# Kernel optimization log

Hardware: AMD Instinct MI355X
Metric: run time of the kernel (lower is better)

The kernel has to match this reference:

```python
import jax, jax.numpy as jnp
import numpy as np

N_TOKENS = 8192
D_MODEL = 1024
D_HIDDEN = 4096
N_EXPERTS = 8
TOP_K = 2


def setup_inputs() -> dict:
    key = jax.random.key(0)
    ks = jax.random.split(key, 7)
    s = 0.02
    return {
        "x": jax.random.normal(ks[0], (N_TOKENS, D_MODEL), dtype=jnp.float32),
        "gate_w": jax.random.normal(ks[1], (D_MODEL, N_EXPERTS), dtype=jnp.float32) * s,
        "gate_b": jnp.zeros((N_EXPERTS,), dtype=jnp.float32),
        "w1": jax.random.normal(ks[2], (N_EXPERTS, D_MODEL, D_HIDDEN), dtype=jnp.float32) * s,
        "b1": jnp.zeros((N_EXPERTS, D_HIDDEN), dtype=jnp.float32),
        "w2": jax.random.normal(ks[3], (N_EXPERTS, D_HIDDEN, D_MODEL), dtype=jnp.float32) * s,
        "b2": jnp.zeros((N_EXPERTS, D_MODEL), dtype=jnp.float32),
    }


def reference(x, gate_w, gate_b, w1, b1, w2, b2):
    # Gating: softmax over experts, then top-k routing
    gate_scores = jax.nn.softmax(x @ gate_w + gate_b, axis=-1)        # [N, E]
    topk_vals, topk_idx = jax.lax.top_k(gate_scores, TOP_K)          # [N, K]

    # Combine weights: sum of topk_vals scattered to expert slots
    onehot = jax.nn.one_hot(topk_idx, N_EXPERTS, dtype=x.dtype)      # [N, K, E]
    combine = jnp.einsum('nk,nke->ne', topk_vals, onehot)            # [N, E]

    # Dense expert evaluation (math identical to masked dispatch: unselected
    # experts receive weight 0 in `combine`).
    h = jax.nn.relu(jnp.einsum('nd,edh->neh', x, w1) + b1)           # [N, E, H]
    expert_out = jnp.einsum('neh,ehd->ned', h, w2) + b2              # [N, E, D]
    output = jnp.einsum('ned,ne->nd', expert_out, combine)           # [N, D]

    # Load-balancing loss from routing counts
    load = jnp.sum(onehot, axis=(0, 1))                              # [E]
    load_balancing_loss = jnp.sum((load / jnp.sum(load)) ** 2)
    return output, load_balancing_loss
```

## Files before the change

### kernel.cpp

```cpp
#include <hip/hip_runtime.h>

#define D_MODEL   1024
#define D_HIDDEN  4096
#define N_EXPERTS 8
#define N_TOKENS  8192
#define NASSIGN   (N_TOKENS * 2)
#define PADCAP    (NASSIGN + N_EXPERTS * 128)
#define ROWT      (PADCAP / 128)

typedef unsigned short u16;
typedef __bf16 bf16x8 __attribute__((ext_vector_type(8)));
typedef float  f32x4  __attribute__((ext_vector_type(4)));

__device__ __forceinline__ u16 f2bf(float f) {
  union { float f; unsigned u; } c; c.f = f;
  unsigned u = c.u;
  u = (u + 0x7fffu + ((u >> 16) & 1u)) >> 16;
  return (u16)u;
}

__device__ __forceinline__ void async16(const void* g, void* l) {
  __builtin_amdgcn_global_load_lds(
      (const __attribute__((address_space(1))) unsigned int*)g,
      (__attribute__((address_space(3))) unsigned int*)l, 16, 0, 0);
}

__global__ __launch_bounds__(256) void gating_kernel(
    const float* __restrict__ x, const float* __restrict__ gw,
    const float* __restrict__ gb, int* __restrict__ counts,
    int* __restrict__ tok_idx, float* __restrict__ tok_w)
{
  const int n = blockIdx.x * 4 + (threadIdx.x >> 6);
  const int lane = threadIdx.x & 63;
  float acc[8] = {0.f,0.f,0.f,0.f,0.f,0.f,0.f,0.f};
  for (int d = lane; d < D_MODEL; d += 64) {
    float xv = x[(size_t)n * D_MODEL + d];
    const float4* g = (const float4*)&gw[d * 8];
    float4 g0 = g[0], g1 = g[1];
    acc[0] += xv * g0.x; acc[1] += xv * g0.y; acc[2] += xv * g0.z; acc[3] += xv * g0.w;
    acc[4] += xv * g1.x; acc[5] += xv * g1.y; acc[6] += xv * g1.z; acc[7] += xv * g1.w;
  }
  for (int off = 32; off; off >>= 1)
    #pragma unroll
    for (int e = 0; e < 8; ++e) acc[e] += __shfl_xor(acc[e], off, 64);
  if (lane == 0) {
    float l[8], p[8];
    float m = -1e30f;
    for (int e = 0; e < 8; ++e) { l[e] = acc[e] + gb[e]; m = fmaxf(m, l[e]); }
    float s = 0.f;
    for (int e = 0; e < 8; ++e) { p[e] = expf(l[e] - m); s += p[e]; }
    float inv = 1.f / s;
    for (int e = 0; e < 8; ++e) p[e] *= inv;
    int i0 = 0;
    for (int e = 1; e < 8; ++e) if (p[e] > p[i0]) i0 = e;
    int i1 = (i0 == 0) ? 1 : 0;
    for (int e = 0; e < 8; ++e) if (e != i0 && p[e] > p[i1]) i1 = e;
    tok_idx[2 * n]     = i0;  tok_idx[2 * n + 1] = i1;
    tok_w[2 * n]       = p[i0]; tok_w[2 * n + 1] = p[i1];
    atomicAdd(&counts[i0], 1);
    atomicAdd(&counts[i1], 1);
  }
}

__global__ void finalize_routing(const int* __restrict__ counts,
                                 int* __restrict__ offsets,
                                 float* __restrict__ out_loss)
{
  int off = 0;
  for (int e = 0; e < 8; ++e) {
    offsets[e] = off;
    off += ((counts[e] + 127) >> 7) << 7;
  }
  offsets[8] = off;
  float loss = 0.f;
  for (int e = 0; e < 8; ++e) {
    float f = (float)counts[e] * (1.f / (float)NASSIGN);
    loss += f * f;
  }
  *out_loss = loss;
}

__global__ __launch_bounds__(256) void scatter_kernel(
    const int* __restrict__ tok_idx, const float* __restrict__ tok_w,
    const int* __restrict__ offsets, int* __restrict__ cursors,
    int* __restrict__ assign_token, float* __restrict__ assign_w,
    int* __restrict__ tok_pos)
{
  const int n = blockIdx.x * 256 + threadIdx.x;
  #pragma unroll
  for (int k = 0; k < 2; ++k) {
    int e = tok_idx[n * 2 + k];
    int pos = offsets[e] + atomicAdd(&cursors[e], 1);
    assign_token[pos] = n;
    assign_w[pos] = tok_w[n * 2 + k];
    tok_pos[n * 2 + k] = pos;
  }
}

__global__ __launch_bounds__(256) void convert_x_kernel(
    const float* __restrict__ x, u16* __restrict__ xb)
{
  size_t i = ((size_t)blockIdx.x * 256 + threadIdx.x) * 4;
  float4 v = *(const float4*)&x[i];
  unsigned lo = (unsigned)f2bf(v.x) | ((unsigned)f2bf(v.y) << 16);
  unsigned hi = (unsigned)f2bf(v.z) | ((unsigned)f2bf(v.w) << 16);
  uint2 o; o.x = lo; o.y = hi;
  *(uint2*)&xb[i] = o;
}

__global__ __launch_bounds__(256) void transpose_cvt_kernel(
    const float* __restrict__ in, u16* __restrict__ out, int R, int C)
{
  const int e = blockIdx.z;
  const int c0 = blockIdx.x * 32, r0 = blockIdx.y * 32;
  __shared__ float tile[32][33];
  const int tx = threadIdx.x & 31, ty = threadIdx.x >> 5;
  const float* ip = in + (size_t)e * R * C;
  u16* op = out + (size_t)e * R * C;
  #pragma unroll
  for (int i = 0; i < 4; ++i)
    tile[ty + i * 8][tx] = ip[(size_t)(r0 + ty + i * 8) * C + c0 + tx];
  __syncthreads();
  #pragma unroll
  for (int i = 0; i < 4; ++i)
    op[(size_t)(c0 + ty + i * 8) * R + r0 + tx] = f2bf(tile[tx][ty + i * 8]);
}

__global__ __launch_bounds__(256, 2) void gemm1_kernel(
    const u16* __restrict__ xb, const u16* __restrict__ w1t,
    const float* __restrict__ b1, const int* __restrict__ assign_token,
    const int* __restrict__ offsets, u16* __restrict__ hbuf)
{
  const int rt = blockIdx.x, ct = blockIdx.y;
  if (rt * 128 >= offsets[8]) return;
  int e = 0;
  while (offsets[e + 1] <= rt * 128) ++e;

  __shared__ __align__(16) u16 smem[36864];
  u16* Asm = smem;
  u16* Bsm = smem + 12288;

  const int tid = threadIdx.x;
  const int wave = tid >> 6, lane = tid & 63;

  const int ra0 = tid >> 2,         sa = tid & 3;
  const int ra1 = (tid + 256) >> 2;
  const int sga0 = sa ^ ((ra0 >> 1) & 3);
  const int sga1 = sa ^ ((ra1 >> 1) & 3);
  const long aBase0 = (long)assign_token[rt * 128 + ra0] * D_MODEL + sga0 * 8;
  const long aBase1 = (long)assign_token[rt * 128 + ra1] * D_MODEL + sga1 * 8;

  long bBase[4];
  #pragma unroll
  for (int k = 0; k < 4; ++k) {
    int c = tid + k * 256;
    int r = c >> 2, s = c & 3;
    int sg = s ^ ((r >> 1) & 3);
    bBase[k] = ((long)e * D_HIDDEN + ct * 256 + r) * D_MODEL + sg * 8;
  }

  const int wr = (wave >> 1) * 64;
  const int wc = (wave & 1) * 128;
  f32x4 acc[4][8];
  #pragma unroll
  for (int i = 0; i < 4; ++i)
    #pragma unroll
    for (int j = 0; j < 8; ++j) acc[i][j] = (f32x4){0.f, 0.f, 0.f, 0.f};

  int aoff[4], boff[8];
  #pragma unroll
  for (int i = 0; i < 4; ++i) {
    int row = wr + i * 16 + (lane & 15);
    aoff[i] = row * 32 + (((lane >> 4) ^ ((row >> 1) & 3)) * 8);
  }
  #pragma unroll
  for (int j = 0; j < 8; ++j) {
    int col = wc + j * 16 + (lane & 15);
    boff[j] = col * 32 + (((lane >> 4) ^ ((col >> 1) & 3)) * 8);
  }

  #define STAGE1(bi, k0) do { \
    u16* A_ = Asm + (bi) * 4096; \
    u16* B_ = Bsm + (bi) * 8192; \
    async16(xb  + aBase0   + (k0), A_ + wave * 512); \
    async16(xb  + aBase1   + (k0), A_ + 2048 + wave * 512); \
    async16(w1t + bBase[0] + (k0), B_ + wave * 512); \
    async16(w1t + bBase[1] + (k0), B_ + 2048 + wave * 512); \
    async16(w1t + bBase[2] + (k0), B_ + 4096 + wave * 512); \
    async16(w1t + bBase[3] + (k0), B_ + 6144 + wave * 512); \
  } while (0)

  const int NT = D_MODEL / 32;
  STAGE1(0, 0);
  STAGE1(1, 32);
  int bi = 0;
  for (int t = 0; t < NT; ++t) {
    if (t < NT - 1) asm volatile("s_waitcnt vmcnt(6)" ::: "memory");
    else            asm volatile("s_waitcnt vmcnt(0)" ::: "memory");
    __builtin_amdgcn_s_barrier();
    const u16* A = Asm + bi * 4096;
    const u16* B = Bsm + bi * 8192;
    bf16x8 a[4], b[8];
    #pragma unroll
    for (int i = 0; i < 4; ++i) a[i] = *(const bf16x8*)&A[aoff[i]];
    #pragma unroll
    for (int j = 0; j < 8; ++j) b[j] = *(const bf16x8*)&B[boff[j]];
    __builtin_amdgcn_s_setprio(1);
    #pragma unroll
    for (int i = 0; i < 4; ++i)
      #pragma unroll
      for (int j = 0; j < 8; ++j)
        acc[i][j] = __builtin_amdgcn_mfma_f32_16x16x32_bf16(a[i], b[j], acc[i][j], 0, 0, 0);
    __builtin_amdgcn_s_setprio(0);
    if (t + 2 < NT) {
      int nb = bi + 2; if (nb >= 3) nb -= 3;
      STAGE1(nb, (t + 2) * 32);
    }
    ++bi; if (bi == 3) bi = 0;
  }
  #undef STAGE1

  float bias[8];
  #pragma unroll
  for (int j = 0; j < 8; ++j)
    bias[j] = b1[(size_t)e * D_HIDDEN + ct * 256 + wc + j * 16 + (lane & 15)];

  __syncthreads();
  u16* Hs = smem;
  #pragma unroll
  for (int i = 0; i < 4; ++i)
    #pragma unroll
    for (int j = 0; j < 8; ++j)
      #pragma unroll
      for (int r = 0; r < 4; ++r) {
        int rl = wr + i * 16 + ((lane >> 4) * 4) + r;
        int cl = wc + j * 16 + (lane & 15);
        Hs[rl * 256 + cl] = f2bf(fmaxf(acc[i][j][r] + bias[j], 0.f));
      }
  __syncthreads();
  #pragma unroll
  for (int t = 0; t < 16; ++t) {
    int cc = tid + t * 256;
    int row = cc >> 5, cs = cc & 31;
    *(uint4*)&hbuf[((size_t)(rt * 128 + row)) * D_HIDDEN + ct * 256 + cs * 8] =
        *(const uint4*)&Hs[row * 256 + cs * 8];
  }
}

template <bool EO>
__global__ __launch_bounds__(256, 2) void gemm2_kernel(
    const u16* __restrict__ hbuf, const u16* __restrict__ w2t,
    const float* __restrict__ b2, const int* __restrict__ assign_token,
    const float* __restrict__ assign_w, const int* __restrict__ offsets,
    float* __restrict__ dst)
{
  const int rt = blockIdx.x, ct = blockIdx.y;
  if (rt * 128 >= offsets[8]) return;
  int e = 0;
  while (offsets[e + 1] <= rt * 128) ++e;

  __shared__ __align__(16) u16 smem[36864];
  u16* Asm = smem;
  u16* Bsm = smem + 12288;
  __shared__ int tokS[128];
  __shared__ float wS[128];

  const int tid = threadIdx.x;
  const int wave = tid >> 6, lane = tid & 63;
  if (tid < 128) {
    tokS[tid] = assign_token[rt * 128 + tid];
    wS[tid] = assign_w[rt * 128 + tid];
  }

  const int ra0 = tid >> 2,         sa = tid & 3;
  const int ra1 = (tid + 256) >> 2;
  const int sga0 = sa ^ ((ra0 >> 1) & 3);
  const int sga1 = sa ^ ((ra1 >> 1) & 3);
  const long aBase0 = ((long)(rt * 128 + ra0)) * D_HIDDEN + sga0 * 8;
  const long aBase1 = ((long)(rt * 128 + ra1)) * D_HIDDEN + sga1 * 8;

  long bBase[4];
  #pragma unroll
  for (int k = 0; k < 4; ++k) {
    int c = tid + k * 256;
    int r = c >> 2, s = c & 3;
    int sg = s ^ ((r >> 1) & 3);
    bBase[k] = ((long)e * D_MODEL + ct * 256 + r) * D_HIDDEN + sg * 8;
  }

  const int wr = (wave >> 1) * 64;
  const int wc = (wave & 1) * 128;
  f32x4 acc[4][8];
  #pragma unroll
  for (int i = 0; i < 4; ++i)
    #pragma unroll
    for (int j = 0; j < 8; ++j) acc[i][j] = (f32x4){0.f, 0.f, 0.f, 0.f};

  int aoff[4], boff[8];
  #pragma unroll
  for (int i = 0; i < 4; ++i) {
    int row = wr + i * 16 + (lane & 15);
    aoff[i] = row * 32 + (((lane >> 4) ^ ((row >> 1) & 3)) * 8);
  }
  #pragma unroll
  for (int j = 0; j < 8; ++j) {
    int col = wc + j * 16 + (lane & 15);
    boff[j] = col * 32 + (((lane >> 4) ^ ((col >> 1) & 3)) * 8);
  }

  #define STAGE2(bi, k0) do { \
    u16* A_ = Asm + (bi) * 4096; \
    u16* B_ = Bsm + (bi) * 8192; \
    async16(hbuf + aBase0   + (k0), A_ + wave * 512); \
    async16(hbuf + aBase1   + (k0), A_ + 2048 + wave * 512); \
    async16(w2t  + bBase[0] + (k0), B_ + wave * 512); \
    async16(w2t  + bBase[1] + (k0), B_ + 2048 + wave * 512); \
    async16(w2t  + bBase[2] + (k0), B_ + 4096 + wave * 512); \
    async16(w2t  + bBase[3] + (k0), B_ + 6144 + wave * 512); \
  } while (0)

  const int NT = D_HIDDEN / 32;
  STAGE2(0, 0);
  STAGE2(1, 32);
  int bi = 0;
  for (int t = 0; t < NT; ++t) {
    if (t < NT - 1) asm volatile("s_waitcnt vmcnt(6)" ::: "memory");
    else            asm volatile("s_waitcnt vmcnt(0)" ::: "memory");
    __builtin_amdgcn_s_barrier();
    const u16* A = Asm + bi * 4096;
    const u16* B = Bsm + bi * 8192;
    bf16x8 a[4], b[8];
    #pragma unroll
    for (int i = 0; i < 4; ++i) a[i] = *(const bf16x8*)&A[aoff[i]];
    #pragma unroll
    for (int j = 0; j < 8; ++j) b[j] = *(const bf16x8*)&B[boff[j]];
    __builtin_amdgcn_s_setprio(1);
    #pragma unroll
    for (int i = 0; i < 4; ++i)
      #pragma unroll
      for (int j = 0; j < 8; ++j)
        acc[i][j] = __builtin_amdgcn_mfma_f32_16x16x32_bf16(a[i], b[j], acc[i][j], 0, 0, 0);
    __builtin_amdgcn_s_setprio(0);
    if (t + 2 < NT) {
      int nb = bi + 2; if (nb >= 3) nb -= 3;
      STAGE2(nb, (t + 2) * 32);
    }
    ++bi; if (bi == 3) bi = 0;
  }
  #undef STAGE2

  float bias[8];
  #pragma unroll
  for (int j = 0; j < 8; ++j)
    bias[j] = b2[(size_t)e * D_MODEL + ct * 256 + wc + j * 16 + (lane & 15)];

  #pragma unroll
  for (int i = 0; i < 4; ++i)
    #pragma unroll
    for (int r = 0; r < 4; ++r) {
      int rl = wr + i * 16 + ((lane >> 4) * 4) + r;
      float wgt = wS[rl];
      if (EO) {
        size_t row = (size_t)(rt * 128 + rl);
        #pragma unroll
        for (int j = 0; j < 8; ++j) {
          float v = (acc[i][j][r] + bias[j]) * wgt;
          dst[row * D_MODEL + ct * 256 + wc + j * 16 + (lane & 15)] = v;
        }
      } else {
        int tok = tokS[rl];
        #pragma unroll
        for (int j = 0; j < 8; ++j) {
          float v = (acc[i][j][r] + bias[j]) * wgt;
          atomicAdd(&dst[(size_t)tok * D_MODEL + ct * 256 + wc + j * 16 + (lane & 15)], v);
        }
      }
    }
}

__global__ __launch_bounds__(256) void combine_kernel(
    const float* __restrict__ eo, const int* __restrict__ tok_pos,
    float* __restrict__ out)
{
  int idx = blockIdx.x * 256 + threadIdx.x;
  int n = idx >> 8;
  int c = (idx & 255) * 4;
  int p0 = tok_pos[2 * n], p1 = tok_pos[2 * n + 1];
  float4 a = *(const float4*)&eo[(size_t)p0 * D_MODEL + c];
  float4 b = *(const float4*)&eo[(size_t)p1 * D_MODEL + c];
  float4 o; o.x = a.x + b.x; o.y = a.y + b.y; o.z = a.z + b.z; o.w = a.w + b.w;
  *(float4*)&out[(size_t)n * D_MODEL + c] = o;
}

__global__ __launch_bounds__(256) void moe_fallback_kernel(
    const float* __restrict__ x, const float* __restrict__ w1,
    const float* __restrict__ b1, const float* __restrict__ w2,
    const float* __restrict__ b2, const int* __restrict__ tok_idx,
    const float* __restrict__ tok_w, float* __restrict__ out)
{
  const int a = blockIdx.x;
  const int n = a >> 1, slot = a & 1;
  const int e = tok_idx[n * 2 + slot];
  const float wgt = tok_w[n * 2 + slot];
  __shared__ float xs[D_MODEL];
  __shared__ float hs[D_HIDDEN];
  const int tid = threadIdx.x;
  for (int d = tid; d < D_MODEL; d += 256) xs[d] = x[(size_t)n * D_MODEL + d];
  __syncthreads();
  for (int h = tid; h < D_HIDDEN; h += 256) {
    float acc = b1[(size_t)e * D_HIDDEN + h];
    for (int d = 0; d < D_MODEL; ++d)
      acc += xs[d] * w1[((size_t)e * D_MODEL + d) * D_HIDDEN + h];
    hs[h] = fmaxf(acc, 0.f);
  }
  __syncthreads();
  for (int d = tid; d < D_MODEL; d += 256) {
    float acc = b2[(size_t)e * D_MODEL + d];
    for (int h = 0; h < D_HIDDEN; ++h)
      acc += hs[h] * w2[((size_t)e * D_HIDDEN + h) * D_MODEL + d];
    atomicAdd(&out[(size_t)n * D_MODEL + d], wgt * acc);
  }
}

extern "C" void kernel_launch(void* const* d_in, const int* in_sizes, int n_in,
                              void* d_out, int out_size, void* d_ws, size_t ws_size,
                              hipStream_t stream) {
  const float* x      = (const float*)d_in[0];
  const float* gate_w = (const float*)d_in[1];
  const float* gate_b = (const float*)d_in[2];
  const float* w1     = (const float*)d_in[3];
  const float* b1     = (const float*)d_in[4];
  const float* w2     = (const float*)d_in[5];
  const float* b2     = (const float*)d_in[6];
  float* out = (float*)d_out;

  char* ws = (char*)d_ws;
  int*   counts       = (int*)(ws + 0);
  int*   cursors      = (int*)(ws + 32);
  int*   offsets      = (int*)(ws + 64);
  int*   tok_idx      = (int*)(ws + 256);
  float* tok_w        = (float*)(ws + 65792);
  int*   tok_pos      = (int*)(ws + 131328);
  int*   assign_token = (int*)(ws + 196864);
  float* assign_w     = (float*)(ws + 266496);
  const size_t X0 = 336128;
  u16* xb   = (u16*)(ws + X0);
  u16* w1t  = (u16*)(ws + X0 + 16777216);
  u16* w2t  = (u16*)(ws + X0);
  u16* hbuf = (u16*)(ws + X0 + 83886080);
  float* eo = (float*)(ws + X0 + 226492416ull);
  const size_t REQ_FAST = X0 + 226492416ull;
  const size_t REQ_EO   = REQ_FAST + 71303168ull;

  const bool fast = (ws_size >= REQ_FAST);
  const bool eoPath = (ws_size >= REQ_EO);

  hipMemsetAsync(ws, 0, fast ? X0 : 336128, stream);
  if (!eoPath) {
    hipMemsetAsync(d_out, 0, (size_t)out_size * sizeof(float), stream);
  }

  gating_kernel<<<N_TOKENS / 4, 256, 0, stream>>>(x, gate_w, gate_b, counts, tok_idx, tok_w);
  finalize_routing<<<1, 1, 0, stream>>>(counts, offsets, out + (out_size - 1));

  if (fast) {
    scatter_kernel<<<N_TOKENS / 256, 256, 0, stream>>>(tok_idx, tok_w, offsets, cursors,
                                                       assign_token, assign_w, tok_pos);
    convert_x_kernel<<<(N_TOKENS * D_MODEL) / 1024, 256, 0, stream>>>(x, xb);
    transpose_cvt_kernel<<<dim3(D_HIDDEN / 32, D_MODEL / 32, N_EXPERTS), 256, 0, stream>>>(
        w1, w1t, D_MODEL, D_HIDDEN);
    gemm1_kernel<<<dim3(ROWT, D_HIDDEN / 256), 256, 0, stream>>>(
        xb, w1t, b1, assign_token, offsets, hbuf);
    transpose_cvt_kernel<<<dim3(D_MODEL / 32, D_HIDDEN / 32, N_EXPERTS), 256, 0, stream>>>(
        w2, w2t, D_HIDDEN, D_MODEL);
    if (eoPath) {
      gemm2_kernel<true><<<dim3(ROWT, D_MODEL / 256), 256, 0, stream>>>(
          hbuf, w2t, b2, assign_token, assign_w, offsets, eo);
      combine_kernel<<<(N_TOKENS * D_MODEL) / 1024, 256, 0, stream>>>(eo, tok_pos, out);
    } else {
      gemm2_kernel<false><<<dim3(ROWT, D_MODEL / 256), 256, 0, stream>>>(
          hbuf, w2t, b2, assign_token, assign_w, offsets, out);
    }
  } else {
    moe_fallback_kernel<<<NASSIGN, 256, 0, stream>>>(x, w1, b1, w2, b2, tok_idx, tok_w, out);
  }
}
```

Baseline: 817.4 us.

## Fuse x bf16 conversion into gating, widen weight transpose, remap GEMM row tiles

The bf16 conversion of x moves into the gating kernel, which already reads x, so one kernel launch and a full extra read of x go away. The weight transpose-convert kernel now uses 64x64 tiles with float4 loads and 16-byte bf16 stores, cutting memory transactions. Both GEMM kernels remap blockIdx.x to a strided row-tile order, (x&7)*17 + (x>>3), so neighbouring blocks work on different experts. That remap assumes ROWT is exactly 136 (8*17). It holds for these constants but is fragile if they change.

Measured after the change: 749.3 us. -8.3%, faster.

```diff
diff --git a/kernel.cpp b/kernel.cpp
--- a/kernel.cpp
+++ b/kernel.cpp
@@ -28,17 +28,35 @@
 __global__ __launch_bounds__(256) void gating_kernel(
     const float* __restrict__ x, const float* __restrict__ gw,
     const float* __restrict__ gb, int* __restrict__ counts,
-    int* __restrict__ tok_idx, float* __restrict__ tok_w)
+    int* __restrict__ tok_idx, float* __restrict__ tok_w,
+    u16* __restrict__ xb)
 {
   const int n = blockIdx.x * 4 + (threadIdx.x >> 6);
   const int lane = threadIdx.x & 63;
+  const float4* x4 = (const float4*)x;
+  const float4* gw4 = (const float4*)gw;
+
   float acc[8] = {0.f,0.f,0.f,0.f,0.f,0.f,0.f,0.f};
-  for (int d = lane; d < D_MODEL; d += 64) {
-    float xv = x[(size_t)n * D_MODEL + d];
-    const float4* g = (const float4*)&gw[d * 8];
-    float4 g0 = g[0], g1 = g[1];
-    acc[0] += xv * g0.x; acc[1] += xv * g0.y; acc[2] += xv * g0.z; acc[3] += xv * g0.w;
-    acc[4] += xv * g1.x; acc[5] += xv * g1.y; acc[6] += xv * g1.z; acc[7] += xv * g1.w;
+  #pragma unroll
+  for (int cch = 0; cch < 4; ++cch) {
+    const int f4i = cch * 64 + lane;
+    float4 xv = x4[(size_t)n * 256 + f4i];
+
+    uint2 o;
+    o.x = (unsigned)f2bf(xv.x) | ((unsigned)f2bf(xv.y) << 16);
+    o.y = (unsigned)f2bf(xv.z) | ((unsigned)f2bf(xv.w) << 16);
+    *(uint2*)&xb[(size_t)n * D_MODEL + f4i * 4] = o;
+
+    float xr[4] = {xv.x, xv.y, xv.z, xv.w};
+    #pragma unroll
+    for (int r = 0; r < 4; ++r) {
+      int row = f4i * 4 + r;
+      float4 g0 = gw4[row * 2], g1 = gw4[row * 2 + 1];
+      acc[0] += xr[r] * g0.x; acc[1] += xr[r] * g0.y;
+      acc[2] += xr[r] * g0.z; acc[3] += xr[r] * g0.w;
+      acc[4] += xr[r] * g1.x; acc[5] += xr[r] * g1.y;
+      acc[6] += xr[r] * g1.z; acc[7] += xr[r] * g1.w;
+    }
   }
   for (int off = 32; off; off >>= 1)
     #pragma unroll
@@ -97,41 +115,40 @@
   }
 }
 
-__global__ __launch_bounds__(256) void convert_x_kernel(
-    const float* __restrict__ x, u16* __restrict__ xb)
-{
-  size_t i = ((size_t)blockIdx.x * 256 + threadIdx.x) * 4;
-  float4 v = *(const float4*)&x[i];
-  unsigned lo = (unsigned)f2bf(v.x) | ((unsigned)f2bf(v.y) << 16);
-  unsigned hi = (unsigned)f2bf(v.z) | ((unsigned)f2bf(v.w) << 16);
-  uint2 o; o.x = lo; o.y = hi;
-  *(uint2*)&xb[i] = o;
-}
-
 __global__ __launch_bounds__(256) void transpose_cvt_kernel(
     const float* __restrict__ in, u16* __restrict__ out, int R, int C)
 {
   const int e = blockIdx.z;
-  const int c0 = blockIdx.x * 32, r0 = blockIdx.y * 32;
-  __shared__ float tile[32][33];
-  const int tx = threadIdx.x & 31, ty = threadIdx.x >> 5;
+  const int c0 = blockIdx.x * 64, r0 = blockIdx.y * 64;
+  __shared__ float tile[64][65];
+  const int tx = threadIdx.x & 15;
+  const int ty = threadIdx.x >> 4;
   const float* ip = in + (size_t)e * R * C;
   u16* op = out + (size_t)e * R * C;
   #pragma unroll
-  for (int i = 0; i < 4; ++i)
-    tile[ty + i * 8][tx] = ip[(size_t)(r0 + ty + i * 8) * C + c0 + tx];
+  for (int i = 0; i < 4; ++i) {
+    int r = ty + i * 16;
+    float4 v = *(const float4*)&ip[(size_t)(r0 + r) * C + c0 + tx * 4];
+    tile[r][tx * 4 + 0] = v.x; tile[r][tx * 4 + 1] = v.y;
+    tile[r][tx * 4 + 2] = v.z; tile[r][tx * 4 + 3] = v.w;
+  }
   __syncthreads();
-  #pragma unroll
-  for (int i = 0; i < 4; ++i)
-    op[(size_t)(c0 + ty + i * 8) * R + r0 + tx] = f2bf(tile[tx][ty + i * 8]);
-}
+  const int c = threadIdx.x >> 2, seg = threadIdx.x & 3;
+  u16 buf[16];
+  #pragma unroll
+  for (int k = 0; k < 16; ++k) buf[k] = f2bf(tile[seg * 16 + k][c]);
+  *(uint4*)&op[(size_t)(c0 + c) * R + r0 + seg * 16]     = *(const uint4*)&buf[0];
+  *(uint4*)&op[(size_t)(c0 + c) * R + r0 + seg * 16 + 8] = *(const uint4*)&buf[8];
+}
+
 
 __global__ __launch_bounds__(256, 2) void gemm1_kernel(
     const u16* __restrict__ xb, const u16* __restrict__ w1t,
     const float* __restrict__ b1, const int* __restrict__ assign_token,
     const int* __restrict__ offsets, u16* __restrict__ hbuf)
 {
-  const int rt = blockIdx.x, ct = blockIdx.y;
+  const int rt = (blockIdx.x & 7) * 17 + (blockIdx.x >> 3);
+  const int ct = blockIdx.y;
   if (rt * 128 >= offsets[8]) return;
   int e = 0;
   while (offsets[e + 1] <= rt * 128) ++e;
@@ -254,7 +271,8 @@
     const float* __restrict__ assign_w, const int* __restrict__ offsets,
     float* __restrict__ dst)
 {
-  const int rt = blockIdx.x, ct = blockIdx.y;
+  const int rt = (blockIdx.x & 7) * 17 + (blockIdx.x >> 3);
+  const int ct = blockIdx.y;
   if (rt * 128 >= offsets[8]) return;
   int e = 0;
   while (offsets[e + 1] <= rt * 128) ++e;
@@ -460,18 +478,18 @@
     hipMemsetAsync(d_out, 0, (size_t)out_size * sizeof(float), stream);
   }
 
-  gating_kernel<<<N_TOKENS / 4, 256, 0, stream>>>(x, gate_w, gate_b, counts, tok_idx, tok_w);
+  gating_kernel<<<N_TOKENS / 4, 256, 0, stream>>>(x, gate_w, gate_b, counts,
+                                                  tok_idx, tok_w, xb);
   finalize_routing<<<1, 1, 0, stream>>>(counts, offsets, out + (out_size - 1));
 
   if (fast) {
     scatter_kernel<<<N_TOKENS / 256, 256, 0, stream>>>(tok_idx, tok_w, offsets, cursors,
                                                        assign_token, assign_w, tok_pos);
-    convert_x_kernel<<<(N_TOKENS * D_MODEL) / 1024, 256, 0, stream>>>(x, xb);
-    transpose_cvt_kernel<<<dim3(D_HIDDEN / 32, D_MODEL / 32, N_EXPERTS), 256, 0, stream>>>(
+    transpose_cvt_kernel<<<dim3(D_HIDDEN / 64, D_MODEL / 64, N_EXPERTS), 256, 0, stream>>>(
         w1, w1t, D_MODEL, D_HIDDEN);
     gemm1_kernel<<<dim3(ROWT, D_HIDDEN / 256), 256, 0, stream>>>(
         xb, w1t, b1, assign_token, offsets, hbuf);
-    transpose_cvt_kernel<<<dim3(D_MODEL / 32, D_HIDDEN / 32, N_EXPERTS), 256, 0, stream>>>(
+    transpose_cvt_kernel<<<dim3(D_MODEL / 64, D_HIDDEN / 64, N_EXPERTS), 256, 0, stream>>>(
         w2, w2t, D_HIDDEN, D_MODEL);
     if (eoPath) {
       gemm2_kernel<true><<<dim3(ROWT, D_MODEL / 256), 256, 0, stream>>>(
```
